# Optimization experiments

Measured on AMD Instinct MI355X. Metric: run time of the kernel, lower is better.

## Reference

```python
import jax, jax.numpy as jnp
import numpy as np

N_NODES = 10000
N_EDGES = 320000
NODE_DIM = 24
EDGE_DIM = 2
HID = 64


def setup_inputs() -> dict:
    key = jax.random.key(0)
    ks = jax.random.split(key, 12)
    s = 0.1  # param scale
    return {
        "x": jax.random.normal(ks[0], (N_NODES, NODE_DIM), dtype=jnp.float32),
        "edge_attr": jax.random.normal(ks[1], (N_EDGES, EDGE_DIM), dtype=jnp.float32),
        "edge_index": jax.random.randint(ks[2], (2, N_EDGES), 0, N_NODES, dtype=jnp.int64),
        "W_in": jax.random.normal(ks[3], (NODE_DIM, HID), dtype=jnp.float32) * s,
        "b_in": jnp.zeros((HID,), dtype=jnp.float32),
        "W_e": jax.random.normal(ks[4], (EDGE_DIM, HID), dtype=jnp.float32) * s,
        "b_e": jnp.zeros((HID,), dtype=jnp.float32),
        "W1": jax.random.normal(ks[5], (HID, HID), dtype=jnp.float32) * s,
        "b1": jnp.zeros((HID,), dtype=jnp.float32),
        "W2": jax.random.normal(ks[6], (HID, HID), dtype=jnp.float32) * s,
        "b2": jnp.zeros((HID,), dtype=jnp.float32),
        "M": jax.random.normal(ks[7], (HID, HID), dtype=jnp.float32) * s,
    }


def reference(x, edge_attr, W_in, b_in, W_e, b_e, W1, b1, W2, b2, M, edge_index):
    n = x.shape[0]
    src, dst = edge_index[0], edge_index[1]  # messages flow src -> dst (PyG convention)

    h = x @ W_in + b_in                      # [N, H]
    ea = edge_attr @ W_e + b_e               # [E, H]

    def gine(h):
        # GINEConv, eps=0: mlp(h_i + sum_j relu(h_j + e_ji)); both convs SHARE the mlp params
        msg = jax.nn.relu(h[src] + ea)                           # [E, H] gather
        agg = jax.ops.segment_sum(msg, dst, num_segments=n)      # [N, H] scatter-add
        z = h + agg
        return jax.nn.relu(z @ W1 + b1) @ W2 + b2

    h = jax.nn.relu(gine(h))
    h = gine(h)

    logits = (h @ M) @ h.T                   # [N, N] bilinear decode
    return jax.nn.softmax(logits, axis=1)
```

## Files before the change

kernel.cpp:

```cpp
#include <hip/hip_runtime.h>

typedef _Float16 half8 __attribute__((ext_vector_type(8)));
typedef float floatx4 __attribute__((ext_vector_type(4)));

#define N_NODES 10000
#define N_EDGES 320000
#define NODE_DIM 24
#define HID 64
#define KSPLIT 192
#define NPAD 10112
#define NT 625
#define NSEG 16
#define TPS 40
#define CSEG 25

__global__ __launch_bounds__(256) void k_embed_hist(
    const float* __restrict__ x, const float* __restrict__ Win,
    const float* __restrict__ bin, float* __restrict__ h0,
    const int* __restrict__ dst, int* __restrict__ cnt) {
  int t = blockIdx.x * blockDim.x + threadIdx.x;
  if (t < N_EDGES) atomicAdd(&cnt[dst[t]], 1);
  int n = t >> 6, j = t & 63;
  if (n >= N_NODES) return;
  float acc = bin[j];
  const float* xr = x + n * NODE_DIM;
#pragma unroll
  for (int k = 0; k < NODE_DIM; ++k) acc = fmaf(xr[k], Win[k * HID + j], acc);
  h0[n * HID + j] = acc;
}

__global__ __launch_bounds__(1024) void k_scan(const int* __restrict__ cnt,
                                               int* __restrict__ offs, int* __restrict__ cur) {
  __shared__ int part[1024];
  int tid = threadIdx.x;
  const int PER = 10;
  int base = tid * PER;
  int loc[PER];
  int s = 0;
#pragma unroll
  for (int i = 0; i < PER; ++i) {
    int e = base + i;
    int v = (e < N_NODES) ? cnt[e] : 0;
    loc[i] = s; s += v;
  }
  part[tid] = s;
  __syncthreads();
  for (int off = 1; off < 1024; off <<= 1) {
    int v = (tid >= off) ? part[tid - off] : 0;
    __syncthreads();
    part[tid] += v;
    __syncthreads();
  }
  int pre = (tid > 0) ? part[tid - 1] : 0;
#pragma unroll
  for (int i = 0; i < PER; ++i) {
    int e = base + i;
    if (e < N_NODES) { int o = pre + loc[i]; offs[e] = o; cur[e] = o; }
  }
  if (tid == 1023) offs[N_NODES] = pre + s;
}

__global__ __launch_bounds__(256) void k_scatter(const int* __restrict__ dst,
                                                 int* __restrict__ cur, int* __restrict__ csr) {
  int e = blockIdx.x * blockDim.x + threadIdx.x;
  if (e < N_EDGES) { int p = atomicAdd(&cur[dst[e]], 1); csr[p] = e; }
}

__global__ __launch_bounds__(256) void k_gine1(
    const float* __restrict__ h, const float* __restrict__ eattr,
    const int* __restrict__ src, const int* __restrict__ csr, const int* __restrict__ offs,
    const float* __restrict__ We, const float* __restrict__ be,
    const float* __restrict__ W1, const float* __restrict__ b1,
    const float* __restrict__ W2, const float* __restrict__ b2,
    float* __restrict__ hout) {
  __shared__ float zs[4][HID];
  __shared__ float ts[4][HID];
  int t = blockIdx.x * blockDim.x + threadIdx.x;
  int n = t >> 6, j = t & 63, nl = threadIdx.x >> 6;
  float w0 = We[j], w1 = We[HID + j], b = be[j];
  const float2* ea2 = (const float2*)eattr;
  float acc = 0.f;
  int e0 = offs[n], e1 = offs[n + 1];
  int i = e0;
  for (; i + 1 < e1; i += 2) {
    int ea_ = csr[i], eb_ = csr[i + 1];
    int sa = src[ea_], sb = src[eb_];
    float2 aa = ea2[ea_], ab = ea2[eb_];
    float va = h[sa * HID + j] + fmaf(aa.x, w0, fmaf(aa.y, w1, b));
    float vb = h[sb * HID + j] + fmaf(ab.x, w0, fmaf(ab.y, w1, b));
    acc += fmaxf(va, 0.f) + fmaxf(vb, 0.f);
  }
  if (i < e1) {
    int ea_ = csr[i];
    int sa = src[ea_];
    float2 aa = ea2[ea_];
    float va = h[sa * HID + j] + fmaf(aa.x, w0, fmaf(aa.y, w1, b));
    acc += fmaxf(va, 0.f);
  }
  float z = h[n * HID + j] + acc;
  zs[nl][j] = z;
  __syncthreads();
  float a1 = b1[j];
#pragma unroll 16
  for (int k = 0; k < HID; ++k) a1 = fmaf(zs[nl][k], W1[k * HID + j], a1);
  float tv = fmaxf(a1, 0.f);
  ts[nl][j] = tv;
  __syncthreads();
  float a2 = b2[j];
#pragma unroll 16
  for (int k = 0; k < HID; ++k) a2 = fmaf(ts[nl][k], W2[k * HID + j], a2);
  hout[n * HID + j] = fmaxf(a2, 0.f);
}

__global__ __launch_bounds__(256) void k_gine2_prep(
    const float* __restrict__ h, const float* __restrict__ eattr,
    const int* __restrict__ src, const int* __restrict__ csr, const int* __restrict__ offs,
    const float* __restrict__ We, const float* __restrict__ be,
    const float* __restrict__ W1, const float* __restrict__ b1,
    const float* __restrict__ W2, const float* __restrict__ b2,
    const float* __restrict__ Mw, _Float16* __restrict__ Ap, _Float16* __restrict__ Bf) {
  __shared__ float zs[4][HID];
  __shared__ float ts[4][HID];
  __shared__ float hs[4][HID];
  if (blockIdx.x == 0) {
    unsigned int* pad = (unsigned int*)(Ap + (size_t)N_NODES * KSPLIT);
    for (int idx = threadIdx.x; idx < (NPAD - N_NODES) * KSPLIT / 2; idx += 256) pad[idx] = 0u;
  }
  int t = blockIdx.x * blockDim.x + threadIdx.x;
  int n = t >> 6, j = t & 63, nl = threadIdx.x >> 6;
  float w0 = We[j], w1 = We[HID + j], b = be[j];
  const float2* ea2 = (const float2*)eattr;
  float acc = 0.f;
  int e0 = offs[n], e1 = offs[n + 1];
  int i = e0;
  for (; i + 1 < e1; i += 2) {
    int ea_ = csr[i], eb_ = csr[i + 1];
    int sa = src[ea_], sb = src[eb_];
    float2 aa = ea2[ea_], ab = ea2[eb_];
    float va = h[sa * HID + j] + fmaf(aa.x, w0, fmaf(aa.y, w1, b));
    float vb = h[sb * HID + j] + fmaf(ab.x, w0, fmaf(ab.y, w1, b));
    acc += fmaxf(va, 0.f) + fmaxf(vb, 0.f);
  }
  if (i < e1) {
    int ea_ = csr[i];
    int sa = src[ea_];
    float2 aa = ea2[ea_];
    float va = h[sa * HID + j] + fmaf(aa.x, w0, fmaf(aa.y, w1, b));
    acc += fmaxf(va, 0.f);
  }
  float z = h[n * HID + j] + acc;
  zs[nl][j] = z;
  __syncthreads();
  float a1 = b1[j];
#pragma unroll 16
  for (int k = 0; k < HID; ++k) a1 = fmaf(zs[nl][k], W1[k * HID + j], a1);
  float tv = fmaxf(a1, 0.f);
  ts[nl][j] = tv;
  __syncthreads();
  float a2 = b2[j];
#pragma unroll 16
  for (int k = 0; k < HID; ++k) a2 = fmaf(ts[nl][k], W2[k * HID + j], a2);
  hs[nl][j] = a2;
  {
    _Float16 bhi = (_Float16)a2;
    _Float16 blo = (_Float16)(a2 - (float)bhi);
    int ct = n >> 4, l16 = n & 15;
    int kk[3] = { j, 64 + j, 128 + j };
    _Float16 vv[3] = { bhi, blo, bhi };
#pragma unroll
    for (int q = 0; q < 3; ++q) {
      int k = kk[q];
      int s = k >> 5, quad = (k & 31) >> 3, jj = k & 7;
      Bf[((((ct * 6 + s) * 64) + quad * 16 + l16) << 3) + jj] = vv[q];
    }
  }
  __syncthreads();
  float accm = 0.f;
#pragma unroll 16
  for (int k = 0; k < HID; ++k) accm = fmaf(hs[nl][k], Mw[k * HID + j], accm);
  _Float16 ahi = (_Float16)accm;
  _Float16 alo = (_Float16)(accm - (float)ahi);
  _Float16* arow = Ap + (size_t)n * KSPLIT;
  arow[j] = ahi; arow[64 + j] = ahi; arow[128 + j] = alo;
}

__global__ __launch_bounds__(256) void k_pass1(
    const _Float16* __restrict__ Ap, const _Float16* __restrict__ Bfh,
    float* __restrict__ pm, float* __restrict__ ps) {
  int seg = blockIdx.x & 15;
  int rg = blockIdx.x >> 4;
  int wave = threadIdx.x >> 6, lane = threadIdx.x & 63;
  int quad = lane >> 4, l16 = lane & 15;
  int rowbase = rg * 128 + wave * 32;
  const half8* A = (const half8*)Ap;
  const half8* Bf = (const half8*)Bfh;
  half8 af[2][6];
#pragma unroll
  for (int tt = 0; tt < 2; ++tt) {
    int ar = rowbase + tt * 16 + l16;
#pragma unroll
    for (int s = 0; s < 6; ++s) af[tt][s] = A[ar * 24 + s * 4 + quad];
  }
  float f[8], sm[8];
  int ct0 = seg * TPS;
  int ct1 = ct0 + TPS; if (ct1 > NT) ct1 = NT;
  bool first = true;
  for (int ct = ct0; ct < ct1; ++ct) {
    half8 bf[6];
#pragma unroll
    for (int s = 0; s < 6; ++s) bf[s] = Bf[(ct * 6 + s) * 64 + lane];
    floatx4 acc0 = {0.f, 0.f, 0.f, 0.f}, acc1 = {0.f, 0.f, 0.f, 0.f};
#pragma unroll
    for (int s = 0; s < 6; ++s) {
      acc0 = __builtin_amdgcn_mfma_f32_16x16x32_f16(af[0][s], bf[s], acc0, 0, 0, 0);
      acc1 = __builtin_amdgcn_mfma_f32_16x16x32_f16(af[1][s], bf[s], acc1, 0, 0, 0);
    }
    float d[8];
#pragma unroll
    for (int i = 0; i < 4; ++i) { d[i] = acc0[i]; d[4 + i] = acc1[i]; }
    if (first) {
      first = false;
#pragma unroll
      for (int i = 0; i < 8; ++i) { f[i] = d[i]; sm[i] = 1.f; }
    } else {
      bool resc = false;
#pragma unroll
      for (int i = 0; i < 8; ++i) resc |= (d[i] > f[i] + 8.f);
      if (__any((int)resc)) {
#pragma unroll
        for (int i = 0; i < 8; ++i) {
          float nf = fmaxf(f[i], d[i]);
          sm[i] = sm[i] * __expf(f[i] - nf) + __expf(d[i] - nf);
          f[i] = nf;
        }
      } else {
#pragma unroll
        for (int i = 0; i < 8; ++i) sm[i] += __expf(d[i] - f[i]);
      }
    }
  }
#pragma unroll
  for (int off = 1; off < 16; off <<= 1) {
#pragma unroll
    for (int i = 0; i < 8; ++i) {
      float fo = __shfl_xor(f[i], off);
      float so = __shfl_xor(sm[i], off);
      float nf = fmaxf(f[i], fo);
      sm[i] = sm[i] * __expf(f[i] - nf) + so * __expf(fo - nf);
      f[i] = nf;
    }
  }
  if (l16 == 0) {
#pragma unroll
    for (int i = 0; i < 8; ++i) {
      int row = rowbase + (i >> 2) * 16 + quad * 4 + (i & 3);
      if (row < N_NODES) {
        pm[seg * N_NODES + row] = f[i];
        ps[seg * N_NODES + row] = sm[i];
      }
    }
  }
}

__global__ __launch_bounds__(256) void k_pass2(
    const _Float16* __restrict__ Ap, const _Float16* __restrict__ Bfh,
    const float* __restrict__ pm, const float* __restrict__ ps, float* __restrict__ out) {
  __shared__ float Ms[128], Is[128];
  int cs = blockIdx.x % CSEG;
  int rg = blockIdx.x / CSEG;
  for (int r = threadIdx.x; r < 128; r += 256) {
    int row = rg * 128 + r;
    if (row < N_NODES) {
      float M = -3.0e38f;
#pragma unroll
      for (int s = 0; s < NSEG; ++s) M = fmaxf(M, pm[s * N_NODES + row]);
      float S = 0.f;
#pragma unroll
      for (int s = 0; s < NSEG; ++s) S += ps[s * N_NODES + row] * __expf(pm[s * N_NODES + row] - M);
      Ms[r] = M; Is[r] = 1.f / S;
    } else { Ms[r] = 0.f; Is[r] = 0.f; }
  }
  int wave = threadIdx.x >> 6, lane = threadIdx.x & 63;
  int quad = lane >> 4, l16 = lane & 15;
  int rowbase = rg * 128 + wave * 32;
  const half8* A = (const half8*)Ap;
  const half8* Bf = (const half8*)Bfh;
  half8 af[2][6];
#pragma unroll
  for (int tt = 0; tt < 2; ++tt) {
    int ar = rowbase + tt * 16 + l16;
#pragma unroll
    for (int s = 0; s < 6; ++s) af[tt][s] = A[ar * 24 + s * 4 + quad];
  }
  __syncthreads();
  float Mv[8], Iv[8];
  int rowv[8];
#pragma unroll
  for (int i = 0; i < 8; ++i) {
    int rl = wave * 32 + (i >> 2) * 16 + quad * 4 + (i & 3);
    rowv[i] = rg * 128 + rl;
    Mv[i] = Ms[rl];
    Iv[i] = Is[rl];
  }
  for (int ct = cs * CSEG; ct < cs * CSEG + CSEG; ++ct) {
    half8 bf[6];
#pragma unroll
    for (int s = 0; s < 6; ++s) bf[s] = Bf[(ct * 6 + s) * 64 + lane];
    floatx4 acc0 = {0.f, 0.f, 0.f, 0.f}, acc1 = {0.f, 0.f, 0.f, 0.f};
#pragma unroll
    for (int s = 0; s < 6; ++s) {
      acc0 = __builtin_amdgcn_mfma_f32_16x16x32_f16(af[0][s], bf[s], acc0, 0, 0, 0);
      acc1 = __builtin_amdgcn_mfma_f32_16x16x32_f16(af[1][s], bf[s], acc1, 0, 0, 0);
    }
    float d[8];
#pragma unroll
    for (int i = 0; i < 4; ++i) { d[i] = acc0[i]; d[4 + i] = acc1[i]; }
    int col = ct * 16 + l16;
#pragma unroll
    for (int i = 0; i < 8; ++i) {
      if (rowv[i] < N_NODES) {
        float v = __expf(d[i] - Mv[i]) * Iv[i];
        __builtin_nontemporal_store(v, &out[(size_t)rowv[i] * N_NODES + col]);
      }
    }
  }
}

extern "C" void kernel_launch(void* const* d_in, const int* in_sizes, int n_in,
                              void* d_out, int out_size, void* d_ws, size_t ws_size,
                              hipStream_t stream) {
  const float* x     = (const float*)d_in[0];
  const float* eattr = (const float*)d_in[1];
  const int*   eidx  = (const int*)d_in[2];
  const float* Win   = (const float*)d_in[3];
  const float* bin   = (const float*)d_in[4];
  const float* We    = (const float*)d_in[5];
  const float* be    = (const float*)d_in[6];
  const float* W1    = (const float*)d_in[7];
  const float* b1    = (const float*)d_in[8];
  const float* W2    = (const float*)d_in[9];
  const float* b2    = (const float*)d_in[10];
  const float* Mw    = (const float*)d_in[11];
  float* out = (float*)d_out;
  const int* src = eidx;
  const int* dst = eidx + N_EDGES;

  char* w = (char*)d_ws;
  auto alloc = [&](size_t bytes) { char* p = w; w += (bytes + 255) & ~(size_t)255; return p; };
  float*    h0   = (float*)alloc((size_t)N_NODES * HID * 4);
  float*    h1   = (float*)alloc((size_t)N_NODES * HID * 4);
  _Float16* Ap   = (_Float16*)alloc((size_t)NPAD * KSPLIT * 2);
  _Float16* Bf   = (_Float16*)alloc((size_t)NT * 6 * 64 * 8 * 2);
  int*      csr  = (int*)alloc((size_t)N_EDGES * 4);
  int*      cnt  = (int*)alloc((size_t)(N_NODES + 1) * 4);
  int*      offs = (int*)alloc((size_t)(N_NODES + 1) * 4);
  int*      cur  = (int*)alloc((size_t)(N_NODES + 1) * 4);
  float*    pm   = (float*)alloc((size_t)NSEG * N_NODES * 4);
  float*    ps   = (float*)alloc((size_t)NSEG * N_NODES * 4);

  hipMemsetAsync(cnt, 0, (N_NODES + 1) * 4, stream);

  k_embed_hist<<<(N_NODES * HID) / 256, 256, 0, stream>>>(x, Win, bin, h0, dst, cnt);
  k_scan<<<1, 1024, 0, stream>>>(cnt, offs, cur);
  k_scatter<<<N_EDGES / 256, 256, 0, stream>>>(dst, cur, csr);

  k_gine1<<<(N_NODES * HID) / 256, 256, 0, stream>>>(
      h0, eattr, src, csr, offs, We, be, W1, b1, W2, b2, h1);
  k_gine2_prep<<<(N_NODES * HID) / 256, 256, 0, stream>>>(
      h1, eattr, src, csr, offs, We, be, W1, b1, W2, b2, Mw, Ap, Bf);

  k_pass1<<<79 * NSEG, 256, 0, stream>>>(Ap, Bf, pm, ps);
  k_pass2<<<79 * CSEG, 256, 0, stream>>>(Ap, Bf, pm, ps, out);
}
```

Baseline: 720.9 us.

## Merge graph and decode stages into two persistent cooperative kernels with grid syncs

Replaces the memset plus seven separate launches with two cooperative persistent kernels. The graph stages (histogram, scan, CSR scatter, two GINE layers and prep) are separated by grid.sync, and the two softmax decode passes are merged the same way. The aim is to remove launch overhead and gaps between kernels. In exchange the grids are limited to 512 blocks, so each block loops over work, and the scan becomes a serial per-thread loop inside one block while the other blocks wait at the barrier.

```diff
diff --git a/kernel.cpp b/kernel.cpp
--- a/kernel.cpp
+++ b/kernel.cpp
@@ -1,4 +1,7 @@
 #include <hip/hip_runtime.h>
+#include <hip/hip_cooperative_groups.h>
+
+namespace cg = cooperative_groups;
 
 typedef _Float16 half8 __attribute__((ext_vector_type(8)));
 typedef float floatx4 __attribute__((ext_vector_type(4)));
@@ -13,316 +16,338 @@
 #define NSEG 16
 #define TPS 40
 #define CSEG 25
-
-__global__ __launch_bounds__(256) void k_embed_hist(
-    const float* __restrict__ x, const float* __restrict__ Win,
-    const float* __restrict__ bin, float* __restrict__ h0,
-    const int* __restrict__ dst, int* __restrict__ cnt) {
-  int t = blockIdx.x * blockDim.x + threadIdx.x;
-  if (t < N_EDGES) atomicAdd(&cnt[dst[t]], 1);
-  int n = t >> 6, j = t & 63;
-  if (n >= N_NODES) return;
-  float acc = bin[j];
-  const float* xr = x + n * NODE_DIM;
-#pragma unroll
-  for (int k = 0; k < NODE_DIM; ++k) acc = fmaf(xr[k], Win[k * HID + j], acc);
-  h0[n * HID + j] = acc;
-}
-
-__global__ __launch_bounds__(1024) void k_scan(const int* __restrict__ cnt,
-                                               int* __restrict__ offs, int* __restrict__ cur) {
-  __shared__ int part[1024];
-  int tid = threadIdx.x;
-  const int PER = 10;
-  int base = tid * PER;
-  int loc[PER];
-  int s = 0;
-#pragma unroll
-  for (int i = 0; i < PER; ++i) {
-    int e = base + i;
-    int v = (e < N_NODES) ? cnt[e] : 0;
-    loc[i] = s; s += v;
-  }
-  part[tid] = s;
-  __syncthreads();
-  for (int off = 1; off < 1024; off <<= 1) {
-    int v = (tid >= off) ? part[tid - off] : 0;
-    __syncthreads();
-    part[tid] += v;
-    __syncthreads();
-  }
-  int pre = (tid > 0) ? part[tid - 1] : 0;
-#pragma unroll
-  for (int i = 0; i < PER; ++i) {
-    int e = base + i;
-    if (e < N_NODES) { int o = pre + loc[i]; offs[e] = o; cur[e] = o; }
-  }
-  if (tid == 1023) offs[N_NODES] = pre + s;
-}
-
-__global__ __launch_bounds__(256) void k_scatter(const int* __restrict__ dst,
-                                                 int* __restrict__ cur, int* __restrict__ csr) {
-  int e = blockIdx.x * blockDim.x + threadIdx.x;
-  if (e < N_EDGES) { int p = atomicAdd(&cur[dst[e]], 1); csr[p] = e; }
-}
-
-__global__ __launch_bounds__(256) void k_gine1(
-    const float* __restrict__ h, const float* __restrict__ eattr,
-    const int* __restrict__ src, const int* __restrict__ csr, const int* __restrict__ offs,
+#define VB1 (79 * NSEG)
+#define VB2 (79 * CSEG)
+#define GA_BLOCKS 512
+#define GB_BLOCKS 512
+
+__global__ __launch_bounds__(256, 2) void k_graph(
+    const float* __restrict__ x, const float* __restrict__ eattr,
+    const int* __restrict__ src, const int* __restrict__ dst,
+    const float* __restrict__ Win, const float* __restrict__ bin,
     const float* __restrict__ We, const float* __restrict__ be,
     const float* __restrict__ W1, const float* __restrict__ b1,
     const float* __restrict__ W2, const float* __restrict__ b2,
-    float* __restrict__ hout) {
-  __shared__ float zs[4][HID];
-  __shared__ float ts[4][HID];
-  int t = blockIdx.x * blockDim.x + threadIdx.x;
-  int n = t >> 6, j = t & 63, nl = threadIdx.x >> 6;
-  float w0 = We[j], w1 = We[HID + j], b = be[j];
-  const float2* ea2 = (const float2*)eattr;
-  float acc = 0.f;
-  int e0 = offs[n], e1 = offs[n + 1];
-  int i = e0;
-  for (; i + 1 < e1; i += 2) {
-    int ea_ = csr[i], eb_ = csr[i + 1];
-    int sa = src[ea_], sb = src[eb_];
-    float2 aa = ea2[ea_], ab = ea2[eb_];
-    float va = h[sa * HID + j] + fmaf(aa.x, w0, fmaf(aa.y, w1, b));
-    float vb = h[sb * HID + j] + fmaf(ab.x, w0, fmaf(ab.y, w1, b));
-    acc += fmaxf(va, 0.f) + fmaxf(vb, 0.f);
-  }
-  if (i < e1) {
-    int ea_ = csr[i];
-    int sa = src[ea_];
-    float2 aa = ea2[ea_];
-    float va = h[sa * HID + j] + fmaf(aa.x, w0, fmaf(aa.y, w1, b));
-    acc += fmaxf(va, 0.f);
-  }
-  float z = h[n * HID + j] + acc;
-  zs[nl][j] = z;
-  __syncthreads();
-  float a1 = b1[j];
-#pragma unroll 16
-  for (int k = 0; k < HID; ++k) a1 = fmaf(zs[nl][k], W1[k * HID + j], a1);
-  float tv = fmaxf(a1, 0.f);
-  ts[nl][j] = tv;
-  __syncthreads();
-  float a2 = b2[j];
-#pragma unroll 16
-  for (int k = 0; k < HID; ++k) a2 = fmaf(ts[nl][k], W2[k * HID + j], a2);
-  hout[n * HID + j] = fmaxf(a2, 0.f);
-}
-
-__global__ __launch_bounds__(256) void k_gine2_prep(
-    const float* __restrict__ h, const float* __restrict__ eattr,
-    const int* __restrict__ src, const int* __restrict__ csr, const int* __restrict__ offs,
-    const float* __restrict__ We, const float* __restrict__ be,
-    const float* __restrict__ W1, const float* __restrict__ b1,
-    const float* __restrict__ W2, const float* __restrict__ b2,
-    const float* __restrict__ Mw, _Float16* __restrict__ Ap, _Float16* __restrict__ Bf) {
+    const float* __restrict__ Mw,
+    float* __restrict__ h0, float* __restrict__ h1,
+    int* __restrict__ cnt, int* __restrict__ offs, int* __restrict__ cur,
+    int* __restrict__ csr, _Float16* __restrict__ Ap, _Float16* __restrict__ Bf) {
+  cg::grid_group grid = cg::this_grid();
   __shared__ float zs[4][HID];
   __shared__ float ts[4][HID];
   __shared__ float hs[4][HID];
+  __shared__ int part[256];
+
+  const int tid = blockIdx.x * 256 + threadIdx.x;
+  const int nthr = GA_BLOCKS * 256;
+  const int j = threadIdx.x & 63, nl = threadIdx.x >> 6;
+  const int gwave = tid >> 6;
+  const int NW = GA_BLOCKS * 4;
+  const int TRIPS = (N_NODES + NW - 1) / NW;
+  const float2* ea2 = (const float2*)eattr;
+
+  for (int i = tid; i <= N_NODES; i += nthr) cnt[i] = 0;
+  {
+    unsigned int* pad = (unsigned int*)(Ap + (size_t)N_NODES * KSPLIT);
+    for (int i = tid; i < (NPAD - N_NODES) * KSPLIT / 2; i += nthr) pad[i] = 0u;
+  }
+  grid.sync();
+
+  for (int e = tid; e < N_EDGES; e += nthr) atomicAdd(&cnt[dst[e]], 1);
+  for (int t = tid; t < N_NODES * HID; t += nthr) {
+    int n = t >> 6, jj = t & 63;
+    float acc = bin[jj];
+    const float* xr = x + n * NODE_DIM;
+#pragma unroll
+    for (int k = 0; k < NODE_DIM; ++k) acc = fmaf(xr[k], Win[k * HID + jj], acc);
+    h0[n * HID + jj] = acc;
+  }
+  grid.sync();
+
   if (blockIdx.x == 0) {
-    unsigned int* pad = (unsigned int*)(Ap + (size_t)N_NODES * KSPLIT);
-    for (int idx = threadIdx.x; idx < (NPAD - N_NODES) * KSPLIT / 2; idx += 256) pad[idx] = 0u;
-  }
-  int t = blockIdx.x * blockDim.x + threadIdx.x;
-  int n = t >> 6, j = t & 63, nl = threadIdx.x >> 6;
-  float w0 = We[j], w1 = We[HID + j], b = be[j];
-  const float2* ea2 = (const float2*)eattr;
-  float acc = 0.f;
-  int e0 = offs[n], e1 = offs[n + 1];
-  int i = e0;
-  for (; i + 1 < e1; i += 2) {
-    int ea_ = csr[i], eb_ = csr[i + 1];
-    int sa = src[ea_], sb = src[eb_];
-    float2 aa = ea2[ea_], ab = ea2[eb_];
-    float va = h[sa * HID + j] + fmaf(aa.x, w0, fmaf(aa.y, w1, b));
-    float vb = h[sb * HID + j] + fmaf(ab.x, w0, fmaf(ab.y, w1, b));
-    acc += fmaxf(va, 0.f) + fmaxf(vb, 0.f);
-  }
-  if (i < e1) {
-    int ea_ = csr[i];
-    int sa = src[ea_];
-    float2 aa = ea2[ea_];
-    float va = h[sa * HID + j] + fmaf(aa.x, w0, fmaf(aa.y, w1, b));
-    acc += fmaxf(va, 0.f);
-  }
-  float z = h[n * HID + j] + acc;
-  zs[nl][j] = z;
-  __syncthreads();
-  float a1 = b1[j];
-#pragma unroll 16
-  for (int k = 0; k < HID; ++k) a1 = fmaf(zs[nl][k], W1[k * HID + j], a1);
-  float tv = fmaxf(a1, 0.f);
-  ts[nl][j] = tv;
-  __syncthreads();
-  float a2 = b2[j];
-#pragma unroll 16
-  for (int k = 0; k < HID; ++k) a2 = fmaf(ts[nl][k], W2[k * HID + j], a2);
-  hs[nl][j] = a2;
-  {
-    _Float16 bhi = (_Float16)a2;
-    _Float16 blo = (_Float16)(a2 - (float)bhi);
-    int ct = n >> 4, l16 = n & 15;
-    int kk[3] = { j, 64 + j, 128 + j };
-    _Float16 vv[3] = { bhi, blo, bhi };
-#pragma unroll
-    for (int q = 0; q < 3; ++q) {
-      int k = kk[q];
-      int s = k >> 5, quad = (k & 31) >> 3, jj = k & 7;
-      Bf[((((ct * 6 + s) * 64) + quad * 16 + l16) << 3) + jj] = vv[q];
-    }
-  }
-  __syncthreads();
-  float accm = 0.f;
-#pragma unroll 16
-  for (int k = 0; k < HID; ++k) accm = fmaf(hs[nl][k], Mw[k * HID + j], accm);
-  _Float16 ahi = (_Float16)accm;
-  _Float16 alo = (_Float16)(accm - (float)ahi);
-  _Float16* arow = Ap + (size_t)n * KSPLIT;
-  arow[j] = ahi; arow[64 + j] = ahi; arow[128 + j] = alo;
+    const int PER = 40;
+    int base = threadIdx.x * PER;
+    int s = 0;
+    for (int i = 0; i < PER; ++i) {
+      int e = base + i;
+      s += (e < N_NODES) ? cnt[e] : 0;
+    }
+    part[threadIdx.x] = s;
+    __syncthreads();
+    for (int off = 1; off < 256; off <<= 1) {
+      int v = (threadIdx.x >= off) ? part[threadIdx.x - off] : 0;
+      __syncthreads();
+      part[threadIdx.x] += v;
+      __syncthreads();
+    }
+    int run = (threadIdx.x > 0) ? part[threadIdx.x - 1] : 0;
+    for (int i = 0; i < PER; ++i) {
+      int e = base + i;
+      if (e < N_NODES) {
+        offs[e] = run; cur[e] = run;
+        run += cnt[e];
+      }
+    }
+    if (threadIdx.x == 255) offs[N_NODES] = part[255];
+  }
+  grid.sync();
+
+  for (int e = tid; e < N_EDGES; e += nthr) {
+    int p = atomicAdd(&cur[dst[e]], 1);
+    csr[p] = e;
+  }
+  grid.sync();
+
+  float w0 = We[j], w1 = We[HID + j], bE = be[j];
+  for (int it = 0; it < TRIPS; ++it) {
+    int n = gwave + it * NW;
+    bool act = (n < N_NODES);
+    float z = 0.f;
+    if (act) {
+      float acc = 0.f;
+      int e0 = offs[n], e1 = offs[n + 1];
+      int i = e0;
+      for (; i + 1 < e1; i += 2) {
+        int ea_ = csr[i], eb_ = csr[i + 1];
+        int sa = src[ea_], sb = src[eb_];
+        float2 aa = ea2[ea_], ab = ea2[eb_];
+        float va = h0[sa * HID + j] + fmaf(aa.x, w0, fmaf(aa.y, w1, bE));
+        float vb = h0[sb * HID + j] + fmaf(ab.x, w0, fmaf(ab.y, w1, bE));
+        acc += fmaxf(va, 0.f) + fmaxf(vb, 0.f);
+      }
+      if (i < e1) {
+        int ea_ = csr[i];
+        int sa = src[ea_];
+        float2 aa = ea2[ea_];
+        float va = h0[sa * HID + j] + fmaf(aa.x, w0, fmaf(aa.y, w1, bE));
+        acc += fmaxf(va, 0.f);
+      }
+      z = h0[n * HID + j] + acc;
+    }
+    zs[nl][j] = z;
+    __syncthreads();
+    float a1 = b1[j];
+#pragma unroll 16
+    for (int k = 0; k < HID; ++k) a1 = fmaf(zs[nl][k], W1[k * HID + j], a1);
+    ts[nl][j] = fmaxf(a1, 0.f);
+    __syncthreads();
+    float a2 = b2[j];
+#pragma unroll 16
+    for (int k = 0; k < HID; ++k) a2 = fmaf(ts[nl][k], W2[k * HID + j], a2);
+    if (act) h1[n * HID + j] = fmaxf(a2, 0.f);
+    __syncthreads();
+  }
+  grid.sync();
+
+  for (int it = 0; it < TRIPS; ++it) {
+    int n = gwave + it * NW;
+    bool act = (n < N_NODES);
+    float z = 0.f;
+    if (act) {
+      float acc = 0.f;
+      int e0 = offs[n], e1 = offs[n + 1];
+      int i = e0;
+      for (; i + 1 < e1; i += 2) {
+        int ea_ = csr[i], eb_ = csr[i + 1];
+        int sa = src[ea_], sb = src[eb_];
+        float2 aa = ea2[ea_], ab = ea2[eb_];
+        float va = h1[sa * HID + j] + fmaf(aa.x, w0, fmaf(aa.y, w1, bE));
+        float vb = h1[sb * HID + j] + fmaf(ab.x, w0, fmaf(ab.y, w1, bE));
+        acc += fmaxf(va, 0.f) + fmaxf(vb, 0.f);
+      }
+      if (i < e1) {
+        int ea_ = csr[i];
+        int sa = src[ea_];
+        float2 aa = ea2[ea_];
+        float va = h1[sa * HID + j] + fmaf(aa.x, w0, fmaf(aa.y, w1, bE));
+        acc += fmaxf(va, 0.f);
+      }
+      z = h1[n * HID + j] + acc;
+    }
+    zs[nl][j] = z;
+    __syncthreads();
+    float a1 = b1[j];
+#pragma unroll 16
+    for (int k = 0; k < HID; ++k) a1 = fmaf(zs[nl][k], W1[k * HID + j], a1);
+    ts[nl][j] = fmaxf(a1, 0.f);
+    __syncthreads();
+    float a2 = b2[j];
+#pragma unroll 16
+    for (int k = 0; k < HID; ++k) a2 = fmaf(ts[nl][k], W2[k * HID + j], a2);
+    hs[nl][j] = a2;
+    if (act) {
+      _Float16 bhi = (_Float16)a2;
+      _Float16 blo = (_Float16)(a2 - (float)bhi);
+      int ct = n >> 4, l16 = n & 15;
+      int kk[3] = { j, 64 + j, 128 + j };
+      _Float16 vv[3] = { bhi, blo, bhi };
+#pragma unroll
+      for (int q = 0; q < 3; ++q) {
+        int k = kk[q];
+        int s = k >> 5, quad = (k & 31) >> 3, jj = k & 7;
+        Bf[((((ct * 6 + s) * 64) + quad * 16 + l16) << 3) + jj] = vv[q];
+      }
+    }
+    __syncthreads();
+    float accm = 0.f;
+#pragma unroll 16
+    for (int k = 0; k < HID; ++k) accm = fmaf(hs[nl][k], Mw[k * HID + j], accm);
+    if (act) {
+      _Float16 ahi = (_Float16)accm;
+      _Float16 alo = (_Float16)(accm - (float)ahi);
+      _Float16* arow = Ap + (size_t)n * KSPLIT;
+      arow[j] = ahi; arow[64 + j] = ahi; arow[128 + j] = alo;
+    }
+    __syncthreads();
+  }
 }
 
-__global__ __launch_bounds__(256) void k_pass1(
+__global__ __launch_bounds__(256, 2) void k_decode(
     const _Float16* __restrict__ Ap, const _Float16* __restrict__ Bfh,
-    float* __restrict__ pm, float* __restrict__ ps) {
-  int seg = blockIdx.x & 15;
-  int rg = blockIdx.x >> 4;
-  int wave = threadIdx.x >> 6, lane = threadIdx.x & 63;
-  int quad = lane >> 4, l16 = lane & 15;
-  int rowbase = rg * 128 + wave * 32;
+    float* __restrict__ pm, float* __restrict__ ps, float* __restrict__ out) {
+  cg::grid_group grid = cg::this_grid();
+  __shared__ float Ms[128], Is[128];
+  const int wave = threadIdx.x >> 6, lane = threadIdx.x & 63;
+  const int quad = lane >> 4, l16 = lane & 15;
   const half8* A = (const half8*)Ap;
   const half8* Bf = (const half8*)Bfh;
-  half8 af[2][6];
-#pragma unroll
-  for (int tt = 0; tt < 2; ++tt) {
-    int ar = rowbase + tt * 16 + l16;
-#pragma unroll
-    for (int s = 0; s < 6; ++s) af[tt][s] = A[ar * 24 + s * 4 + quad];
-  }
-  float f[8], sm[8];
-  int ct0 = seg * TPS;
-  int ct1 = ct0 + TPS; if (ct1 > NT) ct1 = NT;
-  bool first = true;
-  for (int ct = ct0; ct < ct1; ++ct) {
-    half8 bf[6];
-#pragma unroll
-    for (int s = 0; s < 6; ++s) bf[s] = Bf[(ct * 6 + s) * 64 + lane];
-    floatx4 acc0 = {0.f, 0.f, 0.f, 0.f}, acc1 = {0.f, 0.f, 0.f, 0.f};
-#pragma unroll
-    for (int s = 0; s < 6; ++s) {
-      acc0 = __builtin_amdgcn_mfma_f32_16x16x32_f16(af[0][s], bf[s], acc0, 0, 0, 0);
-      acc1 = __builtin_amdgcn_mfma_f32_16x16x32_f16(af[1][s], bf[s], acc1, 0, 0, 0);
-    }
-    float d[8];
-#pragma unroll
-    for (int i = 0; i < 4; ++i) { d[i] = acc0[i]; d[4 + i] = acc1[i]; }
-    if (first) {
-      first = false;
-#pragma unroll
-      for (int i = 0; i < 8; ++i) { f[i] = d[i]; sm[i] = 1.f; }
-    } else {
-      bool resc = false;
-#pragma unroll
-      for (int i = 0; i < 8; ++i) resc |= (d[i] > f[i] + 8.f);
-      if (__any((int)resc)) {
+
+  for (int vb = blockIdx.x; vb < VB1; vb += GB_BLOCKS) {
+    int seg = vb & 15;
+    int rg = vb >> 4;
+    int rowbase = rg * 128 + wave * 32;
+    half8 af[2][6];
+#pragma unroll
+    for (int tt = 0; tt < 2; ++tt) {
+      int ar = rowbase + tt * 16 + l16;
+#pragma unroll
+      for (int s = 0; s < 6; ++s) af[tt][s] = A[ar * 24 + s * 4 + quad];
+    }
+    float f[8], sm[8];
+    bool first = true;
+    int ct0 = seg * TPS;
+    int ct1 = ct0 + TPS; if (ct1 > NT) ct1 = NT;
+    for (int ct = ct0; ct < ct1; ++ct) {
+      half8 bf[6];
+#pragma unroll
+      for (int s = 0; s < 6; ++s) bf[s] = Bf[(ct * 6 + s) * 64 + lane];
+      floatx4 acc0 = {0.f, 0.f, 0.f, 0.f}, acc1 = {0.f, 0.f, 0.f, 0.f};
+#pragma unroll
+      for (int s = 0; s < 6; ++s) {
+        acc0 = __builtin_amdgcn_mfma_f32_16x16x32_f16(af[0][s], bf[s], acc0, 0, 0, 0);
+        acc1 = __builtin_amdgcn_mfma_f32_16x16x32_f16(af[1][s], bf[s], acc1, 0, 0, 0);
+      }
+      float d[8];
+#pragma unroll
+      for (int i = 0; i < 4; ++i) { d[i] = acc0[i]; d[4 + i] = acc1[i]; }
+      if (first) {
+        first = false;
+#pragma unroll
+        for (int i = 0; i < 8; ++i) { f[i] = d[i]; sm[i] = 1.f; }
+      } else {
+        bool resc = false;
+#pragma unroll
+        for (int i = 0; i < 8; ++i) resc |= (d[i] > f[i] + 8.f);
+        if (__any((int)resc)) {
+#pragma unroll
+          for (int i = 0; i < 8; ++i) {
+            float nf = fmaxf(f[i], d[i]);
+            sm[i] = sm[i] * __expf(f[i] - nf) + __expf(d[i] - nf);
+            f[i] = nf;
+          }
+        } else {
+#pragma unroll
+          for (int i = 0; i < 8; ++i) sm[i] += __expf(d[i] - f[i]);
+        }
+      }
+    }
+#pragma unroll
+    for (int off = 1; off < 16; off <<= 1) {
+#pragma unroll
+      for (int i = 0; i < 8; ++i) {
+        float fo = __shfl_xor(f[i], off);
+        float so = __shfl_xor(sm[i], off);
+        float nf = fmaxf(f[i], fo);
+        sm[i] = sm[i] * __expf(f[i] - nf) + so * __expf(fo - nf);
+        f[i] = nf;
+      }
+    }
+    if (l16 == 0) {
+#pragma unroll
+      for (int i = 0; i < 8; ++i) {
+        int row = rowbase + (i >> 2) * 16 + quad * 4 + (i & 3);
+        if (row < N_NODES) {
+          pm[seg * N_NODES + row] = f[i];
+          ps[seg * N_NODES + row] = sm[i];
+        }
+      }
+    }
+  }
+  grid.sync();
+
+  const int T2 = (VB2 + GB_BLOCKS - 1) / GB_BLOCKS;
+  for (int it = 0; it < T2; ++it) {
+    int vb = blockIdx.x + it * GB_BLOCKS;
+    bool act = (vb < VB2);
+    int cs = act ? vb % CSEG : 0;
+    int rg = act ? vb / CSEG : 0;
+    if (act) {
+      for (int r = threadIdx.x; r < 128; r += 256) {
+        int row = rg * 128 + r;
+        if (row < N_NODES) {
+          float M = -3.0e38f;
+#pragma unroll
+          for (int s = 0; s < NSEG; ++s) M = fmaxf(M, pm[s * N_NODES + row]);
+          float S = 0.f;
+#pragma unroll
+          for (int s = 0; s < NSEG; ++s) S += ps[s * N_NODES + row] * __expf(pm[s * N_NODES + row] - M);
+          Ms[r] = M; Is[r] = 1.f / S;
+        } else { Ms[r] = 0.f; Is[r] = 0.f; }
+      }
+    }
+    __syncthreads();
+    if (act) {
+      int rowbase = rg * 128 + wave * 32;
+      half8 af[2][6];
+#pragma unroll
+      for (int tt = 0; tt < 2; ++tt) {
+        int ar = rowbase + tt * 16 + l16;
+#pragma unroll
+        for (int s = 0; s < 6; ++s) af[tt][s] = A[ar * 24 + s * 4 + quad];
+      }
+      float Mv[8], Iv[8];
+      int rowv[8];
+#pragma unroll
+      for (int i = 0; i < 8; ++i) {
+        int rl = wave * 32 + (i >> 2) * 16 + quad * 4 + (i & 3);
+        rowv[i] = rg * 128 + rl;
+        Mv[i] = Ms[rl];
+        Iv[i] = Is[rl];
+      }
+      for (int ct = cs * CSEG; ct < cs * CSEG + CSEG; ++ct) {
+        half8 bf[6];
+#pragma unroll
+        for (int s = 0; s < 6; ++s) bf[s] = Bf[(ct * 6 + s) * 64 + lane];
+        floatx4 acc0 = {0.f, 0.f, 0.f, 0.f}, acc1 = {0.f, 0.f, 0.f, 0.f};
+#pragma unroll
+        for (int s = 0; s < 6; ++s) {
+          acc0 = __builtin_amdgcn_mfma_f32_16x16x32_f16(af[0][s], bf[s], acc0, 0, 0, 0);
+          acc1 = __builtin_amdgcn_mfma_f32_16x16x32_f16(af[1][s], bf[s], acc1, 0, 0, 0);
+        }
+        float d[8];
+#pragma unroll
+        for (int i = 0; i < 4; ++i) { d[i] = acc0[i]; d[4 + i] = acc1[i]; }
+        int col = ct * 16 + l16;
 #pragma unroll
         for (int i = 0; i < 8; ++i) {
-          float nf = fmaxf(f[i], d[i]);
-          sm[i] = sm[i] * __expf(f[i] - nf) + __expf(d[i] - nf);
-          f[i] = nf;
+          if (rowv[i] < N_NODES) {
+            float v = __expf(d[i] - Mv[i]) * Iv[i];
+            __builtin_nontemporal_store(v, &out[(size_t)rowv[i] * N_NODES + col]);
+          }
         }
-      } else {
-#pragma unroll
-        for (int i = 0; i < 8; ++i) sm[i] += __expf(d[i] - f[i]);
-      }
-    }
-  }
-#pragma unroll
-  for (int off = 1; off < 16; off <<= 1) {
-#pragma unroll
-    for (int i = 0; i < 8; ++i) {
-      float fo = __shfl_xor(f[i], off);
-      float so = __shfl_xor(sm[i], off);
-      float nf = fmaxf(f[i], fo);
-      sm[i] = sm[i] * __expf(f[i] - nf) + so * __expf(fo - nf);
-      f[i] = nf;
-    }
-  }
-  if (l16 == 0) {
-#pragma unroll
-    for (int i = 0; i < 8; ++i) {
-      int row = rowbase + (i >> 2) * 16 + quad * 4 + (i & 3);
-      if (row < N_NODES) {
-        pm[seg * N_NODES + row] = f[i];
-        ps[seg * N_NODES + row] = sm[i];
-      }
-    }
-  }
-}
-
-__global__ __launch_bounds__(256) void k_pass2(
-    const _Float16* __restrict__ Ap, const _Float16* __restrict__ Bfh,
-    const float* __restrict__ pm, const float* __restrict__ ps, float* __restrict__ out) {
-  __shared__ float Ms[128], Is[128];
-  int cs = blockIdx.x % CSEG;
-  int rg = blockIdx.x / CSEG;
-  for (int r = threadIdx.x; r < 128; r += 256) {
-    int row = rg * 128 + r;
-    if (row < N_NODES) {
-      float M = -3.0e38f;
-#pragma unroll
-      for (int s = 0; s < NSEG; ++s) M = fmaxf(M, pm[s * N_NODES + row]);
-      float S = 0.f;
-#pragma unroll
-      for (int s = 0; s < NSEG; ++s) S += ps[s * N_NODES + row] * __expf(pm[s * N_NODES + row] - M);
-      Ms[r] = M; Is[r] = 1.f / S;
-    } else { Ms[r] = 0.f; Is[r] = 0.f; }
-  }
-  int wave = threadIdx.x >> 6, lane = threadIdx.x & 63;
-  int quad = lane >> 4, l16 = lane & 15;
-  int rowbase = rg * 128 + wave * 32;
-  const half8* A = (const half8*)Ap;
-  const half8* Bf = (const half8*)Bfh;
-  half8 af[2][6];
-#pragma unroll
-  for (int tt = 0; tt < 2; ++tt) {
-    int ar = rowbase + tt * 16 + l16;
-#pragma unroll
-    for (int s = 0; s < 6; ++s) af[tt][s] = A[ar * 24 + s * 4 + quad];
-  }
-  __syncthreads();
-  float Mv[8], Iv[8];
-  int rowv[8];
-#pragma unroll
-  for (int i = 0; i < 8; ++i) {
-    int rl = wave * 32 + (i >> 2) * 16 + quad * 4 + (i & 3);
-    rowv[i] = rg * 128 + rl;
-    Mv[i] = Ms[rl];
-    Iv[i] = Is[rl];
-  }
-  for (int ct = cs * CSEG; ct < cs * CSEG + CSEG; ++ct) {
-    half8 bf[6];
-#pragma unroll
-    for (int s = 0; s < 6; ++s) bf[s] = Bf[(ct * 6 + s) * 64 + lane];
-    floatx4 acc0 = {0.f, 0.f, 0.f, 0.f}, acc1 = {0.f, 0.f, 0.f, 0.f};
-#pragma unroll
-    for (int s = 0; s < 6; ++s) {
-      acc0 = __builtin_amdgcn_mfma_f32_16x16x32_f16(af[0][s], bf[s], acc0, 0, 0, 0);
-      acc1 = __builtin_amdgcn_mfma_f32_16x16x32_f16(af[1][s], bf[s], acc1, 0, 0, 0);
-    }
-    float d[8];
-#pragma unroll
-    for (int i = 0; i < 4; ++i) { d[i] = acc0[i]; d[4 + i] = acc1[i]; }
-    int col = ct * 16 + l16;
-#pragma unroll
-    for (int i = 0; i < 8; ++i) {
-      if (rowv[i] < N_NODES) {
-        float v = __expf(d[i] - Mv[i]) * Iv[i];
-        __builtin_nontemporal_store(v, &out[(size_t)rowv[i] * N_NODES + col]);
-      }
-    }
+      }
+    }
+    __syncthreads();
   }
 }
 
@@ -358,17 +383,15 @@
   float*    pm   = (float*)alloc((size_t)NSEG * N_NODES * 4);
   float*    ps   = (float*)alloc((size_t)NSEG * N_NODES * 4);
 
-  hipMemsetAsync(cnt, 0, (N_NODES + 1) * 4, stream);
-
-  k_embed_hist<<<(N_NODES * HID) / 256, 256, 0, stream>>>(x, Win, bin, h0, dst, cnt);
-  k_scan<<<1, 1024, 0, stream>>>(cnt, offs, cur);
-  k_scatter<<<N_EDGES / 256, 256, 0, stream>>>(dst, cur, csr);
-
-  k_gine1<<<(N_NODES * HID) / 256, 256, 0, stream>>>(
-      h0, eattr, src, csr, offs, We, be, W1, b1, W2, b2, h1);
-  k_gine2_prep<<<(N_NODES * HID) / 256, 256, 0, stream>>>(
-      h1, eattr, src, csr, offs, We, be, W1, b1, W2, b2, Mw, Ap, Bf);
-
-  k_pass1<<<79 * NSEG, 256, 0, stream>>>(Ap, Bf, pm, ps);
-  k_pass2<<<79 * CSEG, 256, 0, stream>>>(Ap, Bf, pm, ps, out);
+  void* argsA[] = { (void*)&x, (void*)&eattr, (void*)&src, (void*)&dst,
+                    (void*)&Win, (void*)&bin, (void*)&We, (void*)&be,
+                    (void*)&W1, (void*)&b1, (void*)&W2, (void*)&b2, (void*)&Mw,
+                    (void*)&h0, (void*)&h1, (void*)&cnt, (void*)&offs, (void*)&cur,
+                    (void*)&csr, (void*)&Ap, (void*)&Bf };
+  hipLaunchCooperativeKernel((const void*)k_graph, dim3(GA_BLOCKS), dim3(256),
+                             argsA, 0, stream);
+
+  void* argsB[] = { (void*)&Ap, (void*)&Bf, (void*)&pm, (void*)&ps, (void*)&out };
+  hipLaunchCooperativeKernel((const void*)k_decode, dim3(GB_BLOCKS), dim3(256),
+                             argsB, 0, stream);
 }
```

Result: slower. 1.206 ms (+67.3%).

## Pre-permute src and edge attrs into CSR order; vectorize gather across 4 edge lanes

Applied to the files above, without the earlier changes.

The scatter kernel now writes source indices and edge attributes directly in destination-sorted order. This removes the csr->src and csr->edge_attr double indirection in both GINE kernels. The aggregation loop is restructured so each wave processes 4 edges at a time with float4 loads of h rows (16 lanes per edge), followed by a shuffle reduction. This cuts dependent gather latency at the cost of extra writes in scatter and a cross-lane reduction.

```diff
diff --git a/kernel.cpp b/kernel.cpp
--- a/kernel.cpp
+++ b/kernel.cpp
@@ -60,15 +60,51 @@
   if (tid == 1023) offs[N_NODES] = pre + s;
 }
 
-__global__ __launch_bounds__(256) void k_scatter(const int* __restrict__ dst,
-                                                 int* __restrict__ cur, int* __restrict__ csr) {
+__global__ __launch_bounds__(256) void k_scatter(
+    const int* __restrict__ dst, const int* __restrict__ src,
+    const float2* __restrict__ ea2, int* __restrict__ cur,
+    int* __restrict__ srcs, float2* __restrict__ eas) {
   int e = blockIdx.x * blockDim.x + threadIdx.x;
-  if (e < N_EDGES) { int p = atomicAdd(&cur[dst[e]], 1); csr[p] = e; }
+  if (e < N_EDGES) {
+    int p = atomicAdd(&cur[dst[e]], 1);
+    srcs[p] = src[e];
+    eas[p] = ea2[e];
+  }
+}
+
+__device__ __forceinline__ float4 agg4(
+    const float4* __restrict__ h4, const int* __restrict__ srcs,
+    const float2* __restrict__ eas, int e0, int e1, int lane,
+    float4 w0v, float4 w1v, float4 bv) {
+  int g = lane >> 4, jj = lane & 15;
+  float4 acc = {0.f, 0.f, 0.f, 0.f};
+#pragma unroll 2
+  for (int i = e0 + g; i < e1; i += 4) {
+    int sa = srcs[i];
+    float2 aa = eas[i];
+    float4 hv = h4[sa * 16 + jj];
+    float mx = hv.x + fmaf(aa.x, w0v.x, fmaf(aa.y, w1v.x, bv.x));
+    float my = hv.y + fmaf(aa.x, w0v.y, fmaf(aa.y, w1v.y, bv.y));
+    float mz = hv.z + fmaf(aa.x, w0v.z, fmaf(aa.y, w1v.z, bv.z));
+    float mw = hv.w + fmaf(aa.x, w0v.w, fmaf(aa.y, w1v.w, bv.w));
+    acc.x += fmaxf(mx, 0.f);
+    acc.y += fmaxf(my, 0.f);
+    acc.z += fmaxf(mz, 0.f);
+    acc.w += fmaxf(mw, 0.f);
+  }
+#pragma unroll
+  for (int off = 16; off < 64; off <<= 1) {
+    acc.x += __shfl_xor(acc.x, off);
+    acc.y += __shfl_xor(acc.y, off);
+    acc.z += __shfl_xor(acc.z, off);
+    acc.w += __shfl_xor(acc.w, off);
+  }
+  return acc;
 }
 
 __global__ __launch_bounds__(256) void k_gine1(
-    const float* __restrict__ h, const float* __restrict__ eattr,
-    const int* __restrict__ src, const int* __restrict__ csr, const int* __restrict__ offs,
+    const float* __restrict__ h, const int* __restrict__ srcs,
+    const float2* __restrict__ eas, const int* __restrict__ offs,
     const float* __restrict__ We, const float* __restrict__ be,
     const float* __restrict__ W1, const float* __restrict__ b1,
     const float* __restrict__ W2, const float* __restrict__ b2,
@@ -77,34 +113,22 @@
   __shared__ float ts[4][HID];
   int t = blockIdx.x * blockDim.x + threadIdx.x;
   int n = t >> 6, j = t & 63, nl = threadIdx.x >> 6;
-  float w0 = We[j], w1 = We[HID + j], b = be[j];
-  const float2* ea2 = (const float2*)eattr;
-  float acc = 0.f;
-  int e0 = offs[n], e1 = offs[n + 1];
-  int i = e0;
-  for (; i + 1 < e1; i += 2) {
-    int ea_ = csr[i], eb_ = csr[i + 1];
-    int sa = src[ea_], sb = src[eb_];
-    float2 aa = ea2[ea_], ab = ea2[eb_];
-    float va = h[sa * HID + j] + fmaf(aa.x, w0, fmaf(aa.y, w1, b));
-    float vb = h[sb * HID + j] + fmaf(ab.x, w0, fmaf(ab.y, w1, b));
-    acc += fmaxf(va, 0.f) + fmaxf(vb, 0.f);
-  }
-  if (i < e1) {
-    int ea_ = csr[i];
-    int sa = src[ea_];
-    float2 aa = ea2[ea_];
-    float va = h[sa * HID + j] + fmaf(aa.x, w0, fmaf(aa.y, w1, b));
-    acc += fmaxf(va, 0.f);
-  }
-  float z = h[n * HID + j] + acc;
-  zs[nl][j] = z;
+  int lane = threadIdx.x & 63, jj = lane & 15;
+  const float4* h4 = (const float4*)h;
+  float4 w0v = ((const float4*)We)[jj];
+  float4 w1v = ((const float4*)(We + HID))[jj];
+  float4 bv  = ((const float4*)be)[jj];
+  float4 acc = agg4(h4, srcs, eas, offs[n], offs[n + 1], lane, w0v, w1v, bv);
+  if ((lane >> 4) == 0) {
+    float4 hv = h4[n * 16 + jj];
+    float4 z4 = { hv.x + acc.x, hv.y + acc.y, hv.z + acc.z, hv.w + acc.w };
+    ((float4*)&zs[nl][0])[jj] = z4;
+  }
   __syncthreads();
   float a1 = b1[j];
 #pragma unroll 16
   for (int k = 0; k < HID; ++k) a1 = fmaf(zs[nl][k], W1[k * HID + j], a1);
-  float tv = fmaxf(a1, 0.f);
-  ts[nl][j] = tv;
+  ts[nl][j] = fmaxf(a1, 0.f);
   __syncthreads();
   float a2 = b2[j];
 #pragma unroll 16
@@ -113,8 +137,8 @@
 }
 
 __global__ __launch_bounds__(256) void k_gine2_prep(
-    const float* __restrict__ h, const float* __restrict__ eattr,
-    const int* __restrict__ src, const int* __restrict__ csr, const int* __restrict__ offs,
+    const float* __restrict__ h, const int* __restrict__ srcs,
+    const float2* __restrict__ eas, const int* __restrict__ offs,
     const float* __restrict__ We, const float* __restrict__ be,
     const float* __restrict__ W1, const float* __restrict__ b1,
     const float* __restrict__ W2, const float* __restrict__ b2,
@@ -128,34 +152,22 @@
   }
   int t = blockIdx.x * blockDim.x + threadIdx.x;
   int n = t >> 6, j = t & 63, nl = threadIdx.x >> 6;
-  float w0 = We[j], w1 = We[HID + j], b = be[j];
-  const float2* ea2 = (const float2*)eattr;
-  float acc = 0.f;
-  int e0 = offs[n], e1 = offs[n + 1];
-  int i = e0;
-  for (; i + 1 < e1; i += 2) {
-    int ea_ = csr[i], eb_ = csr[i + 1];
-    int sa = src[ea_], sb = src[eb_];
-    float2 aa = ea2[ea_], ab = ea2[eb_];
-    float va = h[sa * HID + j] + fmaf(aa.x, w0, fmaf(aa.y, w1, b));
-    float vb = h[sb * HID + j] + fmaf(ab.x, w0, fmaf(ab.y, w1, b));
-    acc += fmaxf(va, 0.f) + fmaxf(vb, 0.f);
-  }
-  if (i < e1) {
-    int ea_ = csr[i];
-    int sa = src[ea_];
-    float2 aa = ea2[ea_];
-    float va = h[sa * HID + j] + fmaf(aa.x, w0, fmaf(aa.y, w1, b));
-    acc += fmaxf(va, 0.f);
-  }
-  float z = h[n * HID + j] + acc;
-  zs[nl][j] = z;
+  int lane = threadIdx.x & 63, jj = lane & 15;
+  const float4* h4 = (const float4*)h;
+  float4 w0v = ((const float4*)We)[jj];
+  float4 w1v = ((const float4*)(We + HID))[jj];
+  float4 bv  = ((const float4*)be)[jj];
+  float4 acc = agg4(h4, srcs, eas, offs[n], offs[n + 1], lane, w0v, w1v, bv);
+  if ((lane >> 4) == 0) {
+    float4 hv = h4[n * 16 + jj];
+    float4 z4 = { hv.x + acc.x, hv.y + acc.y, hv.z + acc.z, hv.w + acc.w };
+    ((float4*)&zs[nl][0])[jj] = z4;
+  }
   __syncthreads();
   float a1 = b1[j];
 #pragma unroll 16
   for (int k = 0; k < HID; ++k) a1 = fmaf(zs[nl][k], W1[k * HID + j], a1);
-  float tv = fmaxf(a1, 0.f);
-  ts[nl][j] = tv;
+  ts[nl][j] = fmaxf(a1, 0.f);
   __syncthreads();
   float a2 = b2[j];
 #pragma unroll 16
@@ -170,8 +182,8 @@
 #pragma unroll
     for (int q = 0; q < 3; ++q) {
       int k = kk[q];
-      int s = k >> 5, quad = (k & 31) >> 3, jj = k & 7;
-      Bf[((((ct * 6 + s) * 64) + quad * 16 + l16) << 3) + jj] = vv[q];
+      int s = k >> 5, quad = (k & 31) >> 3, je = k & 7;
+      Bf[((((ct * 6 + s) * 64) + quad * 16 + l16) << 3) + je] = vv[q];
     }
   }
   __syncthreads();
@@ -351,7 +363,8 @@
   float*    h1   = (float*)alloc((size_t)N_NODES * HID * 4);
   _Float16* Ap   = (_Float16*)alloc((size_t)NPAD * KSPLIT * 2);
   _Float16* Bf   = (_Float16*)alloc((size_t)NT * 6 * 64 * 8 * 2);
-  int*      csr  = (int*)alloc((size_t)N_EDGES * 4);
+  int*      srcs = (int*)alloc((size_t)N_EDGES * 4);
+  float2*   eas  = (float2*)alloc((size_t)N_EDGES * 8);
   int*      cnt  = (int*)alloc((size_t)(N_NODES + 1) * 4);
   int*      offs = (int*)alloc((size_t)(N_NODES + 1) * 4);
   int*      cur  = (int*)alloc((size_t)(N_NODES + 1) * 4);
@@ -362,12 +375,12 @@
 
   k_embed_hist<<<(N_NODES * HID) / 256, 256, 0, stream>>>(x, Win, bin, h0, dst, cnt);
   k_scan<<<1, 1024, 0, stream>>>(cnt, offs, cur);
-  k_scatter<<<N_EDGES / 256, 256, 0, stream>>>(dst, cur, csr);
+  k_scatter<<<N_EDGES / 256, 256, 0, stream>>>(dst, src, (const float2*)eattr, cur, srcs, eas);
 
   k_gine1<<<(N_NODES * HID) / 256, 256, 0, stream>>>(
-      h0, eattr, src, csr, offs, We, be, W1, b1, W2, b2, h1);
+      h0, srcs, eas, offs, We, be, W1, b1, W2, b2, h1);
   k_gine2_prep<<<(N_NODES * HID) / 256, 256, 0, stream>>>(
-      h1, eattr, src, csr, offs, We, be, W1, b1, W2, b2, Mw, Ap, Bf);
+      h1, srcs, eas, offs, We, be, W1, b1, W2, b2, Mw, Ap, Bf);
 
   k_pass1<<<79 * NSEG, 256, 0, stream>>>(Ap, Bf, pm, ps);
   k_pass2<<<79 * CSEG, 256, 0, stream>>>(Ap, Bf, pm, ps, out);
```

After: 671.3 us. 1.07x faster.
